# Performance work log

Hardware: AMD Instinct MI355X
Metric: run time of the kernel (lower is better)

## Reference

```python
import jax, jax.numpy as jnp
import numpy as np

# Faithful JAX version of ROIMask_To_Img / paste_mask_in_image (Mask R-CNN paste):
# per box: (mask+1)/2, zero-pad by 1, expand box by (M+2)/M, truncate to int,
# bilinear-resize (align_corners=False, edge-clamped) to the box extent, and
# overwrite-paste into the image canvas; final canvas is mapped to [-1, 1].
# Instead of per-box dynamic-size interpolate + slice assignment, we evaluate the
# bilinear resample densely over the full image grid and mask to the box region
# (same math, jit-compatible, single fused gather-resize-scatter).


def _edge_coords(s, size):
    # torch bilinear align_corners=False with edge clamping
    s = jnp.clip(s, 0.0, size - 1.0)
    i0 = jnp.floor(s)
    t = s - i0
    i0 = i0.astype(jnp.int32)
    i1 = jnp.minimum(i0 + 1, size - 1)
    return i0, i1, t


def _paste_step(im, mask, box):
    # im: [H, W] canvas; mask: [M, M] in [-1,1]; box: [4] float (x0, y0, x1, y1)
    H, W = im.shape
    M = mask.shape[-1]
    Mp = M + 2  # padded mask size
    m = jnp.pad((mask + 1.0) * 0.5, 1)  # expand_masks(padding=1) -> [Mp, Mp]
    scale = (M + 2.0) / M
    w_half = (box[2] - box[0]) * (0.5 * scale)
    h_half = (box[3] - box[1]) * (0.5 * scale)
    x_c = (box[2] + box[0]) * 0.5
    y_c = (box[3] + box[1]) * 0.5
    # expand_boxes then .to(int32) (truncation toward zero, like torch)
    b = jnp.trunc(jnp.stack([x_c - w_half, y_c - h_half,
                             x_c + w_half, y_c + h_half])).astype(jnp.int32)
    w = jnp.maximum(b[2] - b[0] + 1, 1).astype(jnp.float32)
    h = jnp.maximum(b[3] - b[1] + 1, 1).astype(jnp.float32)
    px = jnp.arange(H)
    py = jnp.arange(W)
    # source coords in padded-mask space (align_corners=False)
    sx = (px - b[0] + 0.5) * (Mp / w) - 0.5  # [H]
    sy = (py - b[1] + 0.5) * (Mp / h) - 0.5  # [W]
    x0, x1, tx = _edge_coords(sx, Mp)
    y0, y1, ty = _edge_coords(sy, Mp)
    # separable bilinear: mix rows first ([H, Mp]), then columns ([H, W])
    rowmix = m[x0] * (1.0 - tx)[:, None] + m[x1] * tx[:, None]
    val = rowmix[:, y0] * (1.0 - ty)[None, :] + rowmix[:, y1] * ty[None, :]
    # paste region (overwrite semantics, clipped to the image)
    vx = (px >= b[0]) & (px <= b[2])
    vy = (py >= b[1]) & (py <= b[3])
    return jnp.where(vx[:, None] & vy[None, :], val, im)


def setup_inputs() -> dict:
    key = jax.random.key(0)
    B, N, M, H, W = 32, 16, 28, 1024, 1024
    k1, k2, k3, k4 = jax.random.split(key, 4)
    masks = jax.random.uniform(k1, (B, N, 1, M, M), jnp.float32, -1.0, 1.0)
    # valid boxes inside the image: corner + extent
    p0 = jax.random.uniform(k2, (B, N, 2), jnp.float32, 0.0, H - 64.0)
    ext = jax.random.uniform(k3, (B, N, 2), jnp.float32, 16.0, 200.0)
    p1 = jnp.minimum(p0 + ext, H - 2.0)
    rects = jnp.concatenate([p0, p1], axis=-1)  # [B, N, 4] = (x0, y0, x1, y1)
    instance_mask = jnp.zeros((B, 1, H, W), jnp.float32)
    return {"masks": masks, "rects": rects, "instance_mask": instance_mask}


def reference(masks, rects, instance_mask):
    # masks: [B, N, 1, M, M]; rects: [B, N, 4]; instance_mask: [B, 1, H, W]
    H, W = instance_mask.shape[-2], instance_mask.shape[-1]

    def per_image(masks_b, rects_b):
        im0 = jnp.zeros((H, W), jnp.float32)
        def step(im, xs):
            m, bx = xs
            return _paste_step(im, m, bx), None
        im, _ = jax.lax.scan(step, im0, (masks_b[:, 0], rects_b))
        return im

    im = jax.vmap(per_image)(masks, rects)  # [B, H, W]
    return im[:, None, :, :] * 2.0 - 1.0
```

## Files before the change

kernel.cpp:

```cpp
#include <hip/hip_runtime.h>

constexpr int Bc  = 32;
constexpr int Nc  = 16;
constexpr int Mc  = 28;
constexpr int MPc = 30;
constexpr int Hc  = 1024;
constexpr int Wc  = 1024;
constexpr int NBOX = Bc * Nc;
constexpr int MAXROWS = 224;


__global__ __launch_bounds__(256)
void fill_and_prep_kernel(const float* __restrict__ rects,
                          float4* __restrict__ out, int n4,
                          int4* __restrict__ rectbuf,
                          float2* __restrict__ scalebuf)
{
    if (blockIdx.x == 0) {
        #pragma unroll
        for (int i = 0; i < 2; ++i) {
            const int box = threadIdx.x + i * 256;
            const float* r = rects + box * 4;
            const float x0 = r[0], y0 = r[1], x1 = r[2], y1 = r[3];
            const float hs = 0.5357142857142857f;
            const float w_half = (x1 - x0) * hs;
            const float h_half = (y1 - y0) * hs;
            const float xc = (x1 + x0) * 0.5f;
            const float yc = (y1 + y0) * 0.5f;
            const int ib0 = (int)truncf(xc - w_half);
            const int ib1 = (int)truncf(yc - h_half);
            const int ib2 = (int)truncf(xc + w_half);
            const int ib3 = (int)truncf(yc + h_half);
            rectbuf[box] = make_int4(ib0, ib1, ib2, ib3);
            const float w = fmaxf((float)(ib2 - ib0 + 1), 1.0f);
            const float h = fmaxf((float)(ib3 - ib1 + 1), 1.0f);
            scalebuf[box] = make_float2((float)MPc / w, (float)MPc / h);
        }
    }
    const float4 v = make_float4(-1.0f, -1.0f, -1.0f, -1.0f);
    const int stride = gridDim.x * 256;
    for (int i = blockIdx.x * 256 + threadIdx.x; i < n4; i += stride)
        out[i] = v;
}

__global__ __launch_bounds__(256)
void paste_boxes_kernel(const float* __restrict__ masks,
                        const int4* __restrict__ rectbuf,
                        const float2* __restrict__ scalebuf,
                        float* __restrict__ out)
{
    const int box = blockIdx.x;
    const int b   = box >> 4;
    const int n   = box & (Nc - 1);

    const int4 rc = rectbuf[box];
    const int rlo = max(rc.x, 0);
    const int rhi = min(rc.z, Hc - 1);
    const int row = rlo + (int)blockIdx.y;
    if (row > rhi) return;

    const int clo = max(rc.y, 0);
    const int chi = min(rc.w, Wc - 1);
    if (clo + (int)(threadIdx.x & 0xFFFFFFC0u) > chi) return;
    const int col = clo + (int)threadIdx.x;

    bool covered = false;
    #pragma unroll
    for (int k = 0; k < Nc; ++k) {
        if (k > n) {
            const int4 kc = rectbuf[b * Nc + k];
            if (row >= kc.x && row <= kc.z)
                covered |= (col >= kc.y && col <= kc.w);
        }
    }
    if (col > chi || covered) return;

    const float2 sc = scalebuf[box];

    float sx = ((float)(row - rc.x) + 0.5f) * sc.x - 0.5f;
    sx = fminf(fmaxf(sx, 0.0f), (float)(MPc - 1));
    const int   i0 = (int)floorf(sx);
    const float tx = sx - (float)i0;
    const int   i1 = min(i0 + 1, MPc - 1);

    float sy = ((float)(col - rc.y) + 0.5f) * sc.y - 0.5f;
    sy = fminf(fmaxf(sy, 0.0f), (float)(MPc - 1));
    const int   j0 = (int)floorf(sy);
    const float ty = sy - (float)j0;
    const int   j1 = min(j0 + 1, MPc - 1);

    const float* mp = masks + (size_t)box * (Mc * Mc);
    const bool iok0 = (i0 >= 1) & (i0 <= Mc);
    const bool iok1 = (i1 >= 1) & (i1 <= Mc);
    const bool jok0 = (j0 >= 1) & (j0 <= Mc);
    const bool jok1 = (j1 >= 1) & (j1 <= Mc);
    const float m00 = (iok0 & jok0) ? (mp[(i0-1)*Mc + (j0-1)] + 1.0f) * 0.5f : 0.0f;
    const float m10 = (iok1 & jok0) ? (mp[(i1-1)*Mc + (j0-1)] + 1.0f) * 0.5f : 0.0f;
    const float m01 = (iok0 & jok1) ? (mp[(i0-1)*Mc + (j1-1)] + 1.0f) * 0.5f : 0.0f;
    const float m11 = (iok1 & jok1) ? (mp[(i1-1)*Mc + (j1-1)] + 1.0f) * 0.5f : 0.0f;
    const float a0 = m00 * (1.0f - tx) + m10 * tx;
    const float a1 = m01 * (1.0f - tx) + m11 * tx;
    const float val = (a0 * (1.0f - ty) + a1 * ty) * 2.0f - 1.0f;

    out[(size_t)b * Hc * Wc + (size_t)row * Wc + col] = val;
}

extern "C" void kernel_launch(void* const* d_in, const int* in_sizes, int n_in,
                              void* d_out, int out_size, void* d_ws, size_t ws_size,
                              hipStream_t stream) {
    const float* masks = (const float*)d_in[0];
    const float* rects = (const float*)d_in[1];
    float* out = (float*)d_out;

    int4*   rectbuf  = (int4*)d_ws;
    float2* scalebuf = (float2*)((char*)d_ws + 8192);

    fill_and_prep_kernel<<<2048, 256, 0, stream>>>(rects, (float4*)out,
                                                   out_size / 4, rectbuf, scalebuf);

    dim3 grid2(NBOX, MAXROWS);
    paste_boxes_kernel<<<grid2, 256, 0, stream>>>(masks, rectbuf, scalebuf, out);
}
```

Before: 296.8 us.

## Process 16-row chunks per block with shared-memory row/column coverage bitmasks

Each paste block now handles a chunk of 16 rows instead of a single row, so the grid shrinks from 224 to 14 blocks along y per box. The later-box rectangles are staged in shared memory and turned into per-row and per-column coverage bitmasks, which replaces the per-thread 16-box overlap test with one AND-and-shift. Column interpolation setup (sy, j0, j1, ty) is computed once per thread and reused across the rows of the chunk. The fill kernel's grid is also doubled. In exchange the kernel adds two barriers, each block has less parallelism, and the early-exit that dropped whole wavefronts lying beyond the box's right edge is gone.

```diff
diff --git a/kernel.cpp b/kernel.cpp
--- a/kernel.cpp
+++ b/kernel.cpp
@@ -7,7 +7,8 @@
 constexpr int Hc  = 1024;
 constexpr int Wc  = 1024;
 constexpr int NBOX = Bc * Nc;
-constexpr int MAXROWS = 224;
+constexpr int CHROWS = 16;
+constexpr int MAXCH  = 14;
 
 
 __global__ __launch_bounds__(256)
@@ -56,53 +57,68 @@
     const int4 rc = rectbuf[box];
     const int rlo = max(rc.x, 0);
     const int rhi = min(rc.z, Hc - 1);
-    const int row = rlo + (int)blockIdx.y;
-    if (row > rhi) return;
+    const int r0  = rlo + (int)blockIdx.y * CHROWS;
+    if (r0 > rhi) return;
+    const int r1  = min(r0 + CHROWS - 1, rhi);
+
+    __shared__ int4     s_rect[Nc];
+    __shared__ unsigned s_rmask[CHROWS];
+
+    const int tid = threadIdx.x;
+    if (tid < Nc) s_rect[tid] = rectbuf[b * Nc + tid];
+    __syncthreads();
+
+    if (tid < CHROWS) {
+        const int row = r0 + tid;
+        unsigned m = 0;
+        #pragma unroll
+        for (int k = 0; k < Nc; ++k)
+            if (row >= s_rect[k].x && row <= s_rect[k].z) m |= (1u << k);
+        s_rmask[tid] = m;
+    }
 
     const int clo = max(rc.y, 0);
-    const int chi = min(rc.w, Wc - 1);
-    if (clo + (int)(threadIdx.x & 0xFFFFFFC0u) > chi) return;
-    const int col = clo + (int)threadIdx.x;
-
-    bool covered = false;
-    #pragma unroll
-    for (int k = 0; k < Nc; ++k) {
-        if (k > n) {
-            const int4 kc = rectbuf[b * Nc + k];
-            if (row >= kc.x && row <= kc.z)
-                covered |= (col >= kc.y && col <= kc.w);
-        }
+    const int col = clo + tid;
+    unsigned cmask = 0;
+    if (col < Wc) {
+        #pragma unroll
+        for (int k = 0; k < Nc; ++k)
+            if (col >= s_rect[k].y && col <= s_rect[k].w) cmask |= (1u << k);
     }
-    if (col > chi || covered) return;
-
     const float2 sc = scalebuf[box];
-
-    float sx = ((float)(row - rc.x) + 0.5f) * sc.x - 0.5f;
-    sx = fminf(fmaxf(sx, 0.0f), (float)(MPc - 1));
-    const int   i0 = (int)floorf(sx);
-    const float tx = sx - (float)i0;
-    const int   i1 = min(i0 + 1, MPc - 1);
-
     float sy = ((float)(col - rc.y) + 0.5f) * sc.y - 0.5f;
     sy = fminf(fmaxf(sy, 0.0f), (float)(MPc - 1));
     const int   j0 = (int)floorf(sy);
     const float ty = sy - (float)j0;
     const int   j1 = min(j0 + 1, MPc - 1);
-
-    const float* mp = masks + (size_t)box * (Mc * Mc);
-    const bool iok0 = (i0 >= 1) & (i0 <= Mc);
-    const bool iok1 = (i1 >= 1) & (i1 <= Mc);
     const bool jok0 = (j0 >= 1) & (j0 <= Mc);
     const bool jok1 = (j1 >= 1) & (j1 <= Mc);
-    const float m00 = (iok0 & jok0) ? (mp[(i0-1)*Mc + (j0-1)] + 1.0f) * 0.5f : 0.0f;
-    const float m10 = (iok1 & jok0) ? (mp[(i1-1)*Mc + (j0-1)] + 1.0f) * 0.5f : 0.0f;
-    const float m01 = (iok0 & jok1) ? (mp[(i0-1)*Mc + (j1-1)] + 1.0f) * 0.5f : 0.0f;
-    const float m11 = (iok1 & jok1) ? (mp[(i1-1)*Mc + (j1-1)] + 1.0f) * 0.5f : 0.0f;
-    const float a0 = m00 * (1.0f - tx) + m10 * tx;
-    const float a1 = m01 * (1.0f - tx) + m11 * tx;
-    const float val = (a0 * (1.0f - ty) + a1 * ty) * 2.0f - 1.0f;
+    const float* mp = masks + (size_t)box * (Mc * Mc);
+    __syncthreads();
 
-    out[(size_t)b * Hc * Wc + (size_t)row * Wc + col] = val;
+    float* oimg = out + (size_t)b * Hc * Wc;
+
+    for (int rr = 0; rr <= r1 - r0; ++rr) {
+        const unsigned rm = s_rmask[rr];
+        if (((cmask & rm) >> n) == 1u) {
+            const int row = r0 + rr;
+            float sx = ((float)(row - rc.x) + 0.5f) * sc.x - 0.5f;
+            sx = fminf(fmaxf(sx, 0.0f), (float)(MPc - 1));
+            const int   i0 = (int)floorf(sx);
+            const float tx = sx - (float)i0;
+            const int   i1 = min(i0 + 1, MPc - 1);
+            const bool iok0 = (i0 >= 1) & (i0 <= Mc);
+            const bool iok1 = (i1 >= 1) & (i1 <= Mc);
+            const float m00 = (iok0 & jok0) ? (mp[(i0-1)*Mc + (j0-1)] + 1.0f) * 0.5f : 0.0f;
+            const float m10 = (iok1 & jok0) ? (mp[(i1-1)*Mc + (j0-1)] + 1.0f) * 0.5f : 0.0f;
+            const float m01 = (iok0 & jok1) ? (mp[(i0-1)*Mc + (j1-1)] + 1.0f) * 0.5f : 0.0f;
+            const float m11 = (iok1 & jok1) ? (mp[(i1-1)*Mc + (j1-1)] + 1.0f) * 0.5f : 0.0f;
+            const float a0 = m00 * (1.0f - tx) + m10 * tx;
+            const float a1 = m01 * (1.0f - tx) + m11 * tx;
+            const float val = (a0 * (1.0f - ty) + a1 * ty) * 2.0f - 1.0f;
+            oimg[(size_t)row * Wc + col] = val;
+        }
+    }
 }
 
 extern "C" void kernel_launch(void* const* d_in, const int* in_sizes, int n_in,
@@ -115,9 +131,9 @@
     int4*   rectbuf  = (int4*)d_ws;
     float2* scalebuf = (float2*)((char*)d_ws + 8192);
 
-    fill_and_prep_kernel<<<2048, 256, 0, stream>>>(rects, (float4*)out,
+    fill_and_prep_kernel<<<4096, 256, 0, stream>>>(rects, (float4*)out,
                                                    out_size / 4, rectbuf, scalebuf);
 
-    dim3 grid2(NBOX, MAXROWS);
+    dim3 grid2(NBOX, MAXCH);
     paste_boxes_kernel<<<grid2, 256, 0, stream>>>(masks, rectbuf, scalebuf, out);
 }
```

Result: faster. 249.0 us (-16.1%).
